# Kernel tuning notes

Hardware: AMD Instinct MI355X
Metric: run time of the kernel (lower is better)

Reference implementation:

```python
import jax, jax.numpy as jnp
import numpy as np

IN_SIZE = 784
Z_DIM = 128
K_DIM = 8192
BATCH = 16384
ENC_HIDDEN = [512, 256]          # EncoderMLP default
DEC_SIZES = [Z_DIM, 256, 512, 784]  # DecoderMLP default: [latent, *hidden]


def _linear(x, w, b):
    return x @ w + b


def find_nearest(query, target):
    # Faithful to: sqrt(sum((Q-T)^2, -1)).min(1)[1]; sqrt is monotone so
    # argmin of squared distance is identical. Computed via the GEMM
    # expansion instead of materializing the (N,K,D) broadcast tensor.
    q2 = jnp.sum(query * query, axis=1, keepdims=True)        # [N,1]
    t2 = jnp.sum(target * target, axis=1)                     # [K]
    d2 = q2 - 2.0 * (query @ target.T) + t2[None, :]          # [N,K]
    idx = jnp.argmin(d2, axis=1)
    return target[idx]


def setup_inputs() -> dict:
    key = jax.random.key(0)
    ks = jax.random.split(key, 16)
    s = 0.02
    inp = {"X": jax.random.uniform(ks[0], (BATCH, 1, 28, 28), dtype=jnp.float32)}
    # Encoder: 784 -> 512 -> 256 (mlp blocks, ReLU) -> 128 (plain Linear)
    enc_sizes = [IN_SIZE] + ENC_HIDDEN + [Z_DIM]
    for i, (din, dout) in enumerate(zip(enc_sizes, enc_sizes[1:]), 1):
        inp[f"enc_w{i}"] = s * jax.random.normal(ks[i], (din, dout), dtype=jnp.float32)
        inp[f"enc_b{i}"] = jnp.zeros((dout,), dtype=jnp.float32)
    # Codebook
    inp["codebook"] = jax.random.normal(ks[8], (K_DIM, Z_DIM), dtype=jnp.float32)
    # Decoder: 128 -> 256 -> 512 -> 784 (mlp blocks, ReLU) + sigmoid out
    for i, (din, dout) in enumerate(zip(DEC_SIZES, DEC_SIZES[1:]), 1):
        inp[f"dec_w{i}"] = s * jax.random.normal(ks[8 + i], (din, dout), dtype=jnp.float32)
        inp[f"dec_b{i}"] = jnp.zeros((dout,), dtype=jnp.float32)
    return inp


def reference(X, enc_w1, enc_b1, enc_w2, enc_b2, enc_w3, enc_b3, codebook,
              dec_w1, dec_b1, dec_w2, dec_b2, dec_w3, dec_b3):
    x = X.reshape(-1, IN_SIZE)
    # Encoder (mlp_block = Linear+ReLU, final layer plain Linear)
    h = jax.nn.relu(_linear(x, enc_w1, enc_b1))
    h = jax.nn.relu(_linear(h, enc_w2, enc_b2))
    z_enc = _linear(h, enc_w3, enc_b3)                         # [N, Z]
    # Nearest codebook vector for each encoding
    z_dec = find_nearest(z_enc, codebook)                      # [N, Z]
    # Decoder
    d = jax.nn.relu(_linear(z_dec, dec_w1, dec_b1))
    d = jax.nn.relu(_linear(d, dec_w2, dec_b2))
    d = jax.nn.relu(_linear(d, dec_w3, dec_b3))
    x_recon = jax.nn.sigmoid(d).reshape(-1, 1, 28, 28)
    # Nearest encoding for each codebook vector (for embedding loss)
    z_enc_for_embd = find_nearest(codebook, z_enc)             # [K, Z]
    return (x_recon, z_enc, z_dec, z_enc_for_embd)
```

## Files before the change

### kernel.cpp

```cpp
#include <hip/hip_runtime.h>
#include <math.h>

using u16 = unsigned short;
using u32 = unsigned int;
using u64 = unsigned long long;

typedef __bf16 bf16x8 __attribute__((ext_vector_type(8)));
typedef short  s16x8  __attribute__((ext_vector_type(8)));
typedef float  f32x4  __attribute__((ext_vector_type(4)));

__device__ __forceinline__ float b2f(u16 u){
  union { u32 i; float f; } x; x.i = ((u32)u) << 16; return x.f;
}
__device__ __forceinline__ u16 f2b(float f){
  union { float f; u32 i; } x; x.f = f;
  u32 i = x.i;
  u32 r = (i + 0x7fffu + ((i >> 16) & 1u)) >> 16;
  return (u16)r;
}
__device__ __forceinline__ f32x4 mfma16(s16x8 a, s16x8 b, f32x4 c){
  return __builtin_amdgcn_mfma_f32_16x16x32_bf16(
      __builtin_bit_cast(bf16x8, a), __builtin_bit_cast(bf16x8, b), c, 0, 0, 0);
}
__device__ __forceinline__ u64 shfl_xor_u64(u64 v, int m){
  int lo = __shfl_xor((int)(u32)v, m);
  int hi = __shfl_xor((int)(u32)(v >> 32), m);
  return ((u64)(u32)hi << 32) | (u32)lo;
}
__device__ __forceinline__ u64 umin64(u64 a, u64 b){ return a < b ? a : b; }
__device__ __forceinline__ u64 packmin(float v, int idx){
  u32 b = __float_as_uint(v);
  b = (b & 0x80000000u) ? ~b : (b | 0x80000000u);
  return ((u64)b << 32) | (u32)idx;
}
__device__ __forceinline__ void gload16(const void* g, void* l){
  __builtin_amdgcn_global_load_lds(
      (const __attribute__((address_space(1))) unsigned int*)g,
      (__attribute__((address_space(3))) unsigned int*)l, 16, 0, 0);
}

__global__ __launch_bounds__(256) void canary_k(float* out, float code){
  out[threadIdx.x] = code;
}

__global__ __launch_bounds__(256) void prep_weights(
    const float* __restrict__ w1, const float* __restrict__ w2, const float* __restrict__ w3,
    const float* __restrict__ dw1, const float* __restrict__ dw2, const float* __restrict__ dw3,
    const float* __restrict__ cb,
    u16* __restrict__ o1h, u16* __restrict__ o1l, u16* __restrict__ o2h, u16* __restrict__ o2l,
    u16* __restrict__ o3h, u16* __restrict__ o3l, u16* __restrict__ o4h, u16* __restrict__ o4l,
    u16* __restrict__ o5h, u16* __restrict__ o5l, u16* __restrict__ o6h, u16* __restrict__ o6l,
    u16* __restrict__ cbh, u16* __restrict__ cbl)
{
  size_t o = (size_t)blockIdx.x * 256 + threadIdx.x;
  if (o >= 1155072){
    size_t e = o - 1155072;
    if (e >= 1048576) return;
    float v = cb[e];
    u16 h = f2b(v);
    cbh[e] = h;
    cbl[e] = f2b(v - b2f(h));
    return;
  }
  const float* src; u16 *hi, *lo; int K, N, Kp; size_t base;
  if      (o <  425984){ src=w1;  hi=o1h; lo=o1l; K=784; N=512; Kp=832; base=0; }
  else if (o <  557056){ src=w2;  hi=o2h; lo=o2l; K=512; N=256; Kp=512; base=425984; }
  else if (o <  589824){ src=w3;  hi=o3h; lo=o3l; K=256; N=128; Kp=256; base=557056; }
  else if (o <  622592){ src=dw1; hi=o4h; lo=o4l; K=128; N=256; Kp=128; base=589824; }
  else if (o <  753664){ src=dw2; hi=o5h; lo=o5l; K=256; N=512; Kp=256; base=622592; }
  else                 { src=dw3; hi=o6h; lo=o6l; K=512; N=784; Kp=512; base=753664; }
  size_t e = o - base;
  int n = (int)(e / Kp), kp = (int)(e % Kp);
  u16 h = 0, l = 0;
  if (kp < K){
    float v = src[(size_t)kp * N + n];
    h = f2b(v);
    l = f2b(v - b2f(h));
  }
  hi[e] = h; lo[e] = l;
}

__device__ __forceinline__ void norm_row(const float* __restrict__ src, float* __restrict__ dst){
  const float4* r = (const float4*)src;
  float s = 0.f;
  for (int k = 0; k < 32; k++){
    float4 p = r[k];
    s += p.x * p.x + p.y * p.y + p.z * p.z + p.w * p.w;
  }
  *dst = s;
}

struct __align__(16) SmemGemm {
  u16 Ah[128][72];
  u16 Al[128][72];
  u16 Bh[128][72];
  u16 Bl[128][72];
};

template<int ACT, int OUTP>
__device__ __forceinline__ void gemm_body(
    SmemGemm& sm,
    const float* __restrict__ A, const u16* __restrict__ B0, const u16* __restrict__ B1,
    const float* __restrict__ bias, float* __restrict__ Cf,
    u16* __restrict__ P0, u16* __restrict__ P1,
    int Astr, int KLIM, int Kp, int KT, int N, int nRowsB, int bx, int by)
{
  const int tid = threadIdx.x;
  const int m0 = by * 128, n0 = bx * 128;
  const int wave = tid >> 6, lane = tid & 63;
  const int wm = (wave >> 1) * 64, wn = (wave & 1) * 64;
  const int quad = lane >> 4, l15 = lane & 15;
  f32x4 acc[4][4] = {};

  for (int kt = 0; kt < KT; ++kt){
    const int kb = kt * 64;
    #pragma unroll
    for (int c = 0; c < 8; c++){
      int idx = c * 256 + tid;
      int r = idx >> 4, c4 = (idx & 15) * 4;
      float4 v = make_float4(0.f, 0.f, 0.f, 0.f);
      if (kb + c4 < KLIM)
        v = *(const float4*)(A + (size_t)(m0 + r) * Astr + kb + c4);
      ushort4 h, l;
      h.x = f2b(v.x); l.x = f2b(v.x - b2f(h.x));
      h.y = f2b(v.y); l.y = f2b(v.y - b2f(h.y));
      h.z = f2b(v.z); l.z = f2b(v.z - b2f(h.z));
      h.w = f2b(v.w); l.w = f2b(v.w - b2f(h.w));
      *(ushort4*)&sm.Ah[r][c4] = h;
      *(ushort4*)&sm.Al[r][c4] = l;
    }
    #pragma unroll
    for (int c = 0; c < 4; c++){
      int idx = c * 256 + tid;
      int r = idx >> 3, col = (idx & 7) * 8;
      int rb = n0 + r; rb = rb < nRowsB ? rb : nRowsB - 1;
      *(uint4*)&sm.Bh[r][col] = *(const uint4*)(B0 + (size_t)rb * Kp + kb + col);
      *(uint4*)&sm.Bl[r][col] = *(const uint4*)(B1 + (size_t)rb * Kp + kb + col);
    }
    __syncthreads();
    #pragma unroll
    for (int kh = 0; kh < 2; ++kh){
      s16x8 ah[4], al[4], bh[4], bl[4];
      #pragma unroll
      for (int t4 = 0; t4 < 4; t4++){
        ah[t4] = *(const s16x8*)&sm.Ah[wm + t4 * 16 + l15][kh * 32 + quad * 8];
        al[t4] = *(const s16x8*)&sm.Al[wm + t4 * 16 + l15][kh * 32 + quad * 8];
        bh[t4] = *(const s16x8*)&sm.Bh[wn + t4 * 16 + l15][kh * 32 + quad * 8];
        bl[t4] = *(const s16x8*)&sm.Bl[wn + t4 * 16 + l15][kh * 32 + quad * 8];
      }
      #pragma unroll
      for (int mt = 0; mt < 4; mt++)
        #pragma unroll
        for (int nt = 0; nt < 4; nt++){
          acc[mt][nt] = mfma16(ah[mt], bh[nt], acc[mt][nt]);
          acc[mt][nt] = mfma16(ah[mt], bl[nt], acc[mt][nt]);
          acc[mt][nt] = mfma16(al[mt], bh[nt], acc[mt][nt]);
        }
    }
    __syncthreads();
  }

  float bvs[4]; int cols[4];
  #pragma unroll
  for (int nt = 0; nt < 4; nt++){
    int cN = n0 + wn + nt * 16 + l15;
    cols[nt] = cN;
    int cc = cN < N ? cN : N - 1;
    bvs[nt] = bias[cc];
  }
  #pragma unroll
  for (int mt = 0; mt < 4; mt++){
    int rbase = m0 + wm + mt * 16 + quad * 4;
    #pragma unroll
    for (int nt = 0; nt < 4; nt++){
      if (cols[nt] < N){
        #pragma unroll
        for (int r = 0; r < 4; r++){
          float v = acc[mt][nt][r] + bvs[nt];
          if (ACT >= 1) v = v > 0.f ? v : 0.f;
          if (ACT == 2) v = 1.f / (1.f + expf(-v));
          size_t off = (size_t)(rbase + r) * N + cols[nt];
          if (OUTP == 2){
            P0[off] = f2b(v);
          } else {
            Cf[off] = v;
            if (OUTP == 1){
              u16 h = f2b(v);
              P0[off] = h;
              P1[off] = f2b(v - b2f(h));
            }
          }
        }
      }
    }
  }
}

template<int ACT, int OUTP>
__global__ __launch_bounds__(256, 2) void gemm_k(
    const float* __restrict__ A, const u16* __restrict__ B0, const u16* __restrict__ B1,
    const float* __restrict__ bias, float* __restrict__ Cf,
    u16* __restrict__ P0, u16* __restrict__ P1,
    int Astr, int KLIM, int Kp, int KT, int N, int nRowsB)
{
  __shared__ SmemGemm sm;
  gemm_body<ACT, OUTP>(sm, A, B0, B1, bias, Cf, P0, P1, Astr, KLIM, Kp, KT, N, nRowsB,
                       blockIdx.x, blockIdx.y);
}

__global__ __launch_bounds__(256, 2) void fused1(
    const float* __restrict__ X,  const u16* __restrict__ W1h, const u16* __restrict__ W1l,
    const float* __restrict__ b1, float* __restrict__ h1,
    const float* __restrict__ cb, const u16* __restrict__ D1h, const u16* __restrict__ D1l,
    const float* __restrict__ db1, float* __restrict__ g1, float* __restrict__ t2f)
{
  __shared__ SmemGemm sm;
  int bid = blockIdx.x;
  if (bid < 512){
    gemm_body<1,0>(sm, X, W1h, W1l, b1, h1, nullptr, nullptr, 784, 784, 832, 13, 512, 512,
                   bid & 3, bid >> 2);
  } else if (bid < 640){
    int b = bid - 512;
    gemm_body<1,0>(sm, cb, D1h, D1l, db1, g1, nullptr, nullptr, 128, 128, 128, 2, 256, 256,
                   b & 1, b >> 1);
  } else {
    int r = (bid - 640) * 256 + threadIdx.x;
    norm_row(cb + (size_t)r * 128, t2f + r);
  }
}

__global__ __launch_bounds__(256, 2) void fused3(
    const float* __restrict__ h2, const u16* __restrict__ W3h, const u16* __restrict__ W3l,
    const float* __restrict__ b3, float* __restrict__ zenc,
    u16* __restrict__ zhi, u16* __restrict__ zlo,
    const float* __restrict__ g1, const u16* __restrict__ D2h, const u16* __restrict__ D2l,
    const float* __restrict__ db2, float* __restrict__ g2)
{
  __shared__ SmemGemm sm;
  int bid = blockIdx.x;
  if (bid < 128){
    gemm_body<0,1>(sm, h2, W3h, W3l, b3, zenc, zhi, zlo, 256, 256, 256, 4, 128, 128,
                   0, bid);
  } else {
    int b = bid - 128;
    gemm_body<1,0>(sm, g1, D2h, D2l, db2, g2, nullptr, nullptr, 256, 256, 256, 4, 512, 512,
                   b & 3, b >> 2);
  }
}

struct __align__(16) DistSmem {
  u16 smem[2][16384];
  u64 colbuf[4][128];
  u64 sRow[2][128];
  float q2s[128];
};

__device__ __forceinline__ void dist_body(
    DistSmem& sm,
    const u16* __restrict__ Zh, const u16* __restrict__ Zl,
    const u16* __restrict__ Bh, const u16* __restrict__ Bl,
    const float* __restrict__ zenc, const float* __restrict__ t2,
    u64* __restrict__ rowp, u64* __restrict__ colp, int strip, int iblk)
{
  const int tid = threadIdx.x;
  const int i0 = iblk * 128;
  const int wave = tid >> 6, lane = tid & 63;
  const int wm = (wave >> 1) * 32, wn = (wave & 1) * 64;
  const int quad = lane >> 4, l15 = lane & 15;

  const int swz = (l15 & 7) << 4;
  const int cof0 = (((quad << 4)     ) ^ swz) >> 1;
  const int cof1 = (((quad << 4) | 64) ^ swz) >> 1;

  if (tid < 128){
    norm_row(zenc + (size_t)(i0 + tid) * 128, &sm.q2s[tid]);
  }

  s16x8 zh[2][2][2], zl[2][2][2];
  #pragma unroll
  for (int kb = 0; kb < 2; kb++)
    #pragma unroll
    for (int kh = 0; kh < 2; kh++)
      #pragma unroll
      for (int mt = 0; mt < 2; mt++){
        size_t off = (size_t)(i0 + wm + mt * 16 + l15) * 128 + kb * 64 + kh * 32 + quad * 8;
        zh[kb][kh][mt] = *(const s16x8*)(Zh + off);
        zl[kb][kh][mt] = *(const s16x8*)(Zl + off);
      }

  #define STAGE(jt_, kb_, buf_) {                                              \
    size_t jb = (size_t)(strip * 2048 + (jt_) * 128) * 128 + (kb_) * 64;       \
    _Pragma("unroll")                                                          \
    for (int c = 0; c < 2; c++){                                               \
      int ci = c * 512 + tid;                                                  \
      int row = ci >> 3;                                                       \
      size_t g = jb + (size_t)row * 128 + (size_t)(((ci & 7) ^ (row & 7)) * 8);\
      u16* lp = &sm.smem[buf_][ci * 8];                                        \
      gload16(Bh + g, lp);                                                     \
      gload16(Bl + g, lp + 8192);                                              \
    }                                                                          \
  }

  #define COMPUTE(buf_, kb_) {                                                 \
    __builtin_amdgcn_s_setprio(1);                                             \
    _Pragma("unroll")                                                          \
    for (int kh = 0; kh < 2; kh++){                                            \
      const int cof = kh ? cof1 : cof0;                                        \
      s16x8 bh[4], bl[4];                                                      \
      _Pragma("unroll")                                                        \
      for (int nt = 0; nt < 4; nt++){                                          \
        int off = (wn + nt * 16 + l15) * 64 + cof;                             \
        bh[nt] = *(const s16x8*)&sm.smem[buf_][off];                           \
        bl[nt] = *(const s16x8*)&sm.smem[buf_][8192 + off];                    \
      }                                                                        \
      _Pragma("unroll")                                                        \
      for (int mt = 0; mt < 2; mt++)                                           \
        _Pragma("unroll")                                                      \
        for (int nt = 0; nt < 4; nt++){                                        \
          acc[mt][nt] = mfma16(zh[kb_][kh][mt], bh[nt], acc[mt][nt]);          \
          acc[mt][nt] = mfma16(zh[kb_][kh][mt], bl[nt], acc[mt][nt]);          \
          acc[mt][nt] = mfma16(zl[kb_][kh][mt], bh[nt], acc[mt][nt]);          \
          acc[mt][nt] = mfma16(zl[kb_][kh][mt], bl[nt], acc[mt][nt]);          \
        }                                                                      \
    }                                                                          \
    __builtin_amdgcn_s_setprio(0);                                             \
  }

  STAGE(0, 0, 0);

  asm volatile("s_waitcnt lgkmcnt(0)" ::: "memory");
  __builtin_amdgcn_s_barrier();

  float qv[2][4];
  #pragma unroll
  for (int mt = 0; mt < 2; mt++)
    #pragma unroll
    for (int r = 0; r < 4; r++)
      qv[mt][r] = sm.q2s[wm + mt * 16 + quad * 4 + r];

  u64 rowm[2][4];
  #pragma unroll
  for (int mt = 0; mt < 2; mt++)
    #pragma unroll
    for (int r = 0; r < 4; r++) rowm[mt][r] = ~0ULL;

  #pragma unroll 1
  for (int jt = 0; jt < 16; ++jt){
    const int j0 = strip * 2048 + jt * 128;
    float t2v[4]; int gj[4];
    #pragma unroll
    for (int nt = 0; nt < 4; nt++){
      gj[nt] = j0 + wn + nt * 16 + l15;
      t2v[nt] = t2[gj[nt]];
    }
    f32x4 acc[2][4] = {};

    STAGE(jt, 1, 1);
    asm volatile("s_waitcnt vmcnt(8)" ::: "memory");
    __builtin_amdgcn_s_barrier();
    COMPUTE(0, 0)
    __builtin_amdgcn_s_barrier();
    if (jt < 15){
      STAGE(jt + 1, 0, 0);
      asm volatile("s_waitcnt vmcnt(4)" ::: "memory");
    } else {
      asm volatile("s_waitcnt vmcnt(0)" ::: "memory");
    }
    __builtin_amdgcn_s_barrier();
    COMPUTE(1, 1)

    #pragma unroll
    for (int mt = 0; mt < 2; mt++){
      #pragma unroll
      for (int r = 0; r < 4; r++){
        float qq = qv[mt][r];
        float rbest = (qq - 2.f * acc[mt][0][r]) + t2v[0];
        int   ridx  = gj[0];
        #pragma unroll
        for (int nt = 1; nt < 4; nt++){
          float v = (qq - 2.f * acc[mt][nt][r]) + t2v[nt];
          if (v < rbest){ rbest = v; ridx = gj[nt]; }
        }
        rowm[mt][r] = umin64(rowm[mt][r], packmin(rbest, ridx));
      }
    }
    #pragma unroll
    for (int nt = 0; nt < 4; nt++){
      float cbest = 3.4e38f; int cidx = 0;
      #pragma unroll
      for (int mt = 0; mt < 2; mt++){
        #pragma unroll
        for (int r = 0; r < 4; r++){
          float vc = (t2v[nt] - 2.f * acc[mt][nt][r]) + qv[mt][r];
          if (vc < cbest){ cbest = vc; cidx = i0 + wm + mt * 16 + quad * 4 + r; }
        }
      }
      u64 p = packmin(cbest, cidx);
      p = umin64(p, shfl_xor_u64(p, 16));
      p = umin64(p, shfl_xor_u64(p, 32));
      if (quad == 0)
        sm.colbuf[wave >> 1][wn + nt * 16 + l15] = p;
    }
    __builtin_amdgcn_s_barrier();
    if (tid < 128){
      u64 p = umin64(umin64(sm.colbuf[0][tid], sm.colbuf[1][tid]),
                     umin64(sm.colbuf[2][tid], sm.colbuf[3][tid]));
      colp[(size_t)iblk * 8192 + j0 + tid] = p;
    }
  }
  #undef STAGE
  #undef COMPUTE

  #pragma unroll
  for (int mt = 0; mt < 2; mt++)
    #pragma unroll
    for (int r = 0; r < 4; r++){
      u64 p = rowm[mt][r];
      p = umin64(p, shfl_xor_u64(p, 1));
      p = umin64(p, shfl_xor_u64(p, 2));
      p = umin64(p, shfl_xor_u64(p, 4));
      p = umin64(p, shfl_xor_u64(p, 8));
      rowm[mt][r] = p;
    }
  if (l15 == 0){
    #pragma unroll
    for (int mt = 0; mt < 2; mt++)
      #pragma unroll
      for (int r = 0; r < 4; r++)
        sm.sRow[wave & 1][wm + mt * 16 + quad * 4 + r] = rowm[mt][r];
  }
  __syncthreads();
  if (tid < 128)
    rowp[(size_t)strip * 16384 + i0 + tid] = umin64(sm.sRow[0][tid], sm.sRow[1][tid]);
}

__global__ __launch_bounds__(512, 2) void dist_k(
    const u16* __restrict__ Zh, const u16* __restrict__ Zl,
    const u16* __restrict__ Bh, const u16* __restrict__ Bl,
    const float* __restrict__ zenc, const float* __restrict__ t2,
    u64* __restrict__ rowp, u64* __restrict__ colp)
{
  __shared__ DistSmem sm;
  dist_body(sm, Zh, Zl, Bh, Bl, zenc, t2, rowp, colp, blockIdx.x & 3, blockIdx.x >> 2);
}

union SmemF5 {
  SmemGemm g;
  struct { u64 s[4][64]; int sidx[64]; } r;
};

__global__ __launch_bounds__(256, 2) void fused5(
    const float* __restrict__ g2, const u16* __restrict__ D3h, const u16* __restrict__ D3l,
    const float* __restrict__ db3, u16* __restrict__ xdecb,
    const u64* __restrict__ rowp, const u64* __restrict__ colp,
    const float* __restrict__ cb, const float* __restrict__ zenc,
    float* __restrict__ zdec, float* __restrict__ zembd, int* __restrict__ rowidx)
{
  __shared__ SmemF5 sm;
  int bid = blockIdx.x;
  if (bid < 448){
    gemm_body<2,2>(sm.g, g2, D3h, D3l, db3, nullptr, xdecb, nullptr,
                   512, 512, 512, 8, 784, 784, bid % 7, bid / 7);
    return;
  }
  bid -= 448;
  int tid = threadIdx.x;
  if (bid < 256){
    int base = bid * 64;
    int n = base + (tid & 63);
    u64 best = ~0ULL;
    for (int p = tid >> 6; p < 4; p += 4)
      best = umin64(best, rowp[(size_t)p * 16384 + n]);
    sm.r.s[tid >> 6][tid & 63] = best;
    __syncthreads();
    if (tid < 64){
      u64 b = umin64(umin64(sm.r.s[0][tid], sm.r.s[1][tid]),
                     umin64(sm.r.s[2][tid], sm.r.s[3][tid]));
      int idx = (int)(b & 0xffffffffULL);
      idx = idx < 0 ? 0 : (idx > 8191 ? 8191 : idx);
      sm.r.sidx[tid] = idx;
      rowidx[base + tid] = idx;
    }
    __syncthreads();
    for (int q = 0; q < 32; q++){
      int e = q * 256 + tid; int r = e >> 7, c = e & 127;
      zdec[(size_t)(base + r) * 128 + c] = cb[(size_t)sm.r.sidx[r] * 128 + c];
    }
  } else {
    int base = (bid - 256) * 64;
    int n = base + (tid & 63);
    u64 best = ~0ULL;
    for (int p = tid >> 6; p < 128; p += 4)
      best = umin64(best, colp[(size_t)p * 8192 + n]);
    sm.r.s[tid >> 6][tid & 63] = best;
    __syncthreads();
    if (tid < 64){
      u64 b = umin64(umin64(sm.r.s[0][tid], sm.r.s[1][tid]),
                     umin64(sm.r.s[2][tid], sm.r.s[3][tid]));
      int idx = (int)(b & 0xffffffffULL);
      idx = idx < 0 ? 0 : (idx > 16383 ? 16383 : idx);
      sm.r.sidx[tid] = idx;
    }
    __syncthreads();
    for (int q = 0; q < 32; q++){
      int e = q * 256 + tid; int r = e >> 7, c = e & 127;
      zembd[(size_t)(base + r) * 128 + c] = zenc[(size_t)sm.r.sidx[r] * 128 + c];
    }
  }
}

__global__ __launch_bounds__(256) void gather_xrec(
    const u16* __restrict__ xdecb, const int* __restrict__ rowidx, float* __restrict__ xrec)
{
  size_t o = (size_t)blockIdx.x * 256 + threadIdx.x;
  int row = (int)(o / 784), c = (int)(o % 784);
  int idx = rowidx[row];
  idx = idx < 0 ? 0 : (idx > 8191 ? 8191 : idx);
  xrec[o] = b2f(xdecb[(size_t)idx * 784 + c]);
}

extern "C" void kernel_launch(void* const* d_in, const int* in_sizes, int n_in,
                              void* d_out, int out_size, void* d_ws, size_t ws_size,
                              hipStream_t stream){
  const float* X   = (const float*)d_in[0];
  const float* w1  = (const float*)d_in[1];  const float* b1  = (const float*)d_in[2];
  const float* w2  = (const float*)d_in[3];  const float* b2  = (const float*)d_in[4];
  const float* w3  = (const float*)d_in[5];  const float* b3  = (const float*)d_in[6];
  const float* cb  = (const float*)d_in[7];
  const float* dw1 = (const float*)d_in[8];  const float* db1 = (const float*)d_in[9];
  const float* dw2 = (const float*)d_in[10]; const float* db2 = (const float*)d_in[11];
  const float* dw3 = (const float*)d_in[12]; const float* db3 = (const float*)d_in[13];

  float* out   = (float*)d_out;
  float* xrec  = out;
  float* zenc  = out + 12845056;
  float* zdec  = zenc + 2097152;
  float* zembd = zdec + 2097152;

  const size_t NEEDED = 22020096;
  if (ws_size < NEEDED){
    canary_k<<<1, 256, 0, stream>>>(out, 1000.0f + (float)(ws_size >> 20));
    return;
  }

  char* ob = (char*)d_out;
  float* h1   = (float*)(ob + 0);
  u16*   zhi  = (u16*)(ob + 8388608);
  u16*   zlo  = (u16*)(ob + 12582912);
  float* g2   = (float*)(ob + 16777216);
  float* g1   = (float*)(ob + 33554432);
  u16*   cbhi = (u16*)(ob + 41943040);
  u16*   cblo = (u16*)(ob + 44040192);
  u64*   colp = (u64*)(ob + 0);

  char* w = (char*)d_ws;
  u16* W1Th = (u16*)(w + 0);        u16* W1Tl = (u16*)(w + 851968);
  u16* W2Th = (u16*)(w + 1703936);  u16* W2Tl = (u16*)(w + 1966080);
  u16* W3Th = (u16*)(w + 2228224);  u16* W3Tl = (u16*)(w + 2293760);
  u16* D1Th = (u16*)(w + 2359296);  u16* D1Tl = (u16*)(w + 2424832);
  u16* D2Th = (u16*)(w + 2490368);  u16* D2Tl = (u16*)(w + 2752512);
  u16* D3Th = (u16*)(w + 3014656);  u16* D3Tl = (u16*)(w + 3817472);
  float* t2f = (float*)(w + 4620288);
  int*  rowi = (int*)(w + 4653056);
  u64*  rowp = (u64*)(w + 4718592);
  float* h2  = (float*)(w + 5242880);
  u16* xdecb = (u16*)(w + 5242880);

  prep_weights<<<8608, 256, 0, stream>>>(w1, w2, w3, dw1, dw2, dw3, cb,
      W1Th, W1Tl, W2Th, W2Tl, W3Th, W3Tl, D1Th, D1Tl, D2Th, D2Tl, D3Th, D3Tl, cbhi, cblo);

  fused1<<<672, 256, 0, stream>>>(X, W1Th, W1Tl, b1, h1, cb, D1Th, D1Tl, db1, g1, t2f);

  gemm_k<1, 0><<<dim3(2, 128), 256, 0, stream>>>(h1, W2Th, W2Tl, b2, h2, nullptr, nullptr,
                                                 512, 512, 512, 8, 256, 256);

  fused3<<<384, 256, 0, stream>>>(h2, W3Th, W3Tl, b3, zenc, zhi, zlo,
                                  g1, D2Th, D2Tl, db2, g2);

  dist_k<<<512, 512, 0, stream>>>(zhi, zlo, cbhi, cblo, zenc, t2f, rowp, colp);

  fused5<<<832, 256, 0, stream>>>(g2, D3Th, D3Tl, db3, xdecb,
                                  rowp, colp, cb, zenc, zdec, zembd, rowi);

  gather_xrec<<<50176, 256, 0, stream>>>(xdecb, rowi, xrec);
}
```

Baseline: 500.1 us.

## Software-pipeline distance epilogue with next tile's MFMA using double accumulators

Splits the tile loop into a ping-pong schedule with two accumulator sets, so the row/column argmin scans for tile j are interleaved with the MFMA work for tile j+1. This is meant to hide the VALU-heavy epilogue (distance evaluation, packing, shuffles, LDS column merge) behind matrix-core work instead of running it serially after each tile. In exchange it doubles accumulator register use, which may raise VGPR pressure and lower occupancy. It also adds explicit prologue and epilogue code.

```diff
diff --git a/kernel.cpp b/kernel.cpp
--- a/kernel.cpp
+++ b/kernel.cpp
@@ -301,7 +301,7 @@
     }                                                                          \
   }
 
-  #define COMPUTE(buf_, kb_) {                                                 \
+  #define COMPUTE(buf_, kb_, ACC) {                                            \
     __builtin_amdgcn_s_setprio(1);                                             \
     _Pragma("unroll")                                                          \
     for (int kh = 0; kh < 2; kh++){                                            \
@@ -317,15 +317,72 @@
       for (int mt = 0; mt < 2; mt++)                                           \
         _Pragma("unroll")                                                      \
         for (int nt = 0; nt < 4; nt++){                                        \
-          acc[mt][nt] = mfma16(zh[kb_][kh][mt], bh[nt], acc[mt][nt]);          \
-          acc[mt][nt] = mfma16(zh[kb_][kh][mt], bl[nt], acc[mt][nt]);          \
-          acc[mt][nt] = mfma16(zl[kb_][kh][mt], bh[nt], acc[mt][nt]);          \
-          acc[mt][nt] = mfma16(zl[kb_][kh][mt], bl[nt], acc[mt][nt]);          \
+          ACC[mt][nt] = mfma16(zh[kb_][kh][mt], bh[nt], ACC[mt][nt]);          \
+          ACC[mt][nt] = mfma16(zh[kb_][kh][mt], bl[nt], ACC[mt][nt]);          \
+          ACC[mt][nt] = mfma16(zl[kb_][kh][mt], bh[nt], ACC[mt][nt]);          \
+          ACC[mt][nt] = mfma16(zl[kb_][kh][mt], bl[nt], ACC[mt][nt]);          \
         }                                                                      \
     }                                                                          \
     __builtin_amdgcn_s_setprio(0);                                             \
   }
 
+  #define LOADT2(T2V, J0_) {                                                   \
+    _Pragma("unroll")                                                          \
+    for (int nt = 0; nt < 4; nt++) T2V[nt] = t2[(J0_) + wn + nt * 16 + l15];   \
+  }
+
+  #define ZEROACC(ACC) {                                                       \
+    _Pragma("unroll")                                                          \
+    for (int mt = 0; mt < 2; mt++)                                             \
+      _Pragma("unroll")                                                        \
+      for (int nt = 0; nt < 4; nt++) ACC[mt][nt] = VZ;                         \
+  }
+
+  #define ROWSCAN(ACC, T2V, J0_) {                                             \
+    _Pragma("unroll")                                                          \
+    for (int mt = 0; mt < 2; mt++){                                            \
+      _Pragma("unroll")                                                        \
+      for (int r = 0; r < 4; r++){                                             \
+        float qq = qv[mt][r];                                                  \
+        float rbest = (qq - 2.f * ACC[mt][0][r]) + T2V[0];                     \
+        int   ridx  = (J0_) + wn + l15;                                        \
+        _Pragma("unroll")                                                      \
+        for (int nt = 1; nt < 4; nt++){                                        \
+          float v = (qq - 2.f * ACC[mt][nt][r]) + T2V[nt];                     \
+          if (v < rbest){ rbest = v; ridx = (J0_) + wn + nt * 16 + l15; }      \
+        }                                                                      \
+        rowm[mt][r] = umin64(rowm[mt][r], packmin(rbest, ridx));               \
+      }                                                                        \
+    }                                                                          \
+  }
+
+  #define COLSCAN(ACC, T2V) {                                                  \
+    _Pragma("unroll")                                                          \
+    for (int nt = 0; nt < 4; nt++){                                            \
+      float cbest = 3.4e38f; int cidx = 0;                                     \
+      _Pragma("unroll")                                                        \
+      for (int mt = 0; mt < 2; mt++){                                          \
+        _Pragma("unroll")                                                      \
+        for (int r = 0; r < 4; r++){                                           \
+          float vc = (T2V[nt] - 2.f * ACC[mt][nt][r]) + qv[mt][r];             \
+          if (vc < cbest){ cbest = vc; cidx = i0 + wm + mt * 16 + quad * 4 + r; } \
+        }                                                                      \
+      }                                                                        \
+      u64 p = packmin(cbest, cidx);                                            \
+      p = umin64(p, shfl_xor_u64(p, 16));                                      \
+      p = umin64(p, shfl_xor_u64(p, 32));                                      \
+      if (quad == 0) sm.colbuf[wave >> 1][wn + nt * 16 + l15] = p;             \
+    }                                                                          \
+  }
+
+  #define MERGECOL(J0_) {                                                      \
+    if (tid < 128){                                                            \
+      u64 p = umin64(umin64(sm.colbuf[0][tid], sm.colbuf[1][tid]),             \
+                     umin64(sm.colbuf[2][tid], sm.colbuf[3][tid]));            \
+      colp[(size_t)iblk * 8192 + (J0_) + tid] = p;                             \
+    }                                                                          \
+  }
+
   STAGE(0, 0, 0);
 
   asm volatile("s_waitcnt lgkmcnt(0)" ::: "memory");
@@ -344,72 +401,92 @@
     #pragma unroll
     for (int r = 0; r < 4; r++) rowm[mt][r] = ~0ULL;
 
+  const f32x4 VZ = {0.f, 0.f, 0.f, 0.f};
+  f32x4 accA[2][4], accB[2][4];
+  float t2vA[4], t2vB[4];
+  int j0A, j0B;
+
+  j0A = strip * 2048;
+  LOADT2(t2vA, j0A);
+  ZEROACC(accA);
+  STAGE(0, 1, 1);
+  asm volatile("s_waitcnt vmcnt(8)" ::: "memory");
+  __builtin_amdgcn_s_barrier();
+  COMPUTE(0, 0, accA)
+  __builtin_amdgcn_s_barrier();
+  STAGE(1, 0, 0);
+  asm volatile("s_waitcnt vmcnt(4)" ::: "memory");
+  __builtin_amdgcn_s_barrier();
+  COMPUTE(1, 1, accA)
+  __builtin_amdgcn_s_barrier();
+
   #pragma unroll 1
-  for (int jt = 0; jt < 16; ++jt){
-    const int j0 = strip * 2048 + jt * 128;
-    float t2v[4]; int gj[4];
-    #pragma unroll
-    for (int nt = 0; nt < 4; nt++){
-      gj[nt] = j0 + wn + nt * 16 + l15;
-      t2v[nt] = t2[gj[nt]];
-    }
-    f32x4 acc[2][4] = {};
-
-    STAGE(jt, 1, 1);
+  for (int jp = 0; jp < 7; ++jp){
+    const int jt1 = 2 * jp + 1;
+    j0B = strip * 2048 + jt1 * 128;
+    LOADT2(t2vB, j0B);
+    ZEROACC(accB);
+    STAGE(jt1, 1, 1);
     asm volatile("s_waitcnt vmcnt(8)" ::: "memory");
     __builtin_amdgcn_s_barrier();
-    COMPUTE(0, 0)
-    __builtin_amdgcn_s_barrier();
-    if (jt < 15){
-      STAGE(jt + 1, 0, 0);
-      asm volatile("s_waitcnt vmcnt(4)" ::: "memory");
-    } else {
-      asm volatile("s_waitcnt vmcnt(0)" ::: "memory");
-    }
-    __builtin_amdgcn_s_barrier();
-    COMPUTE(1, 1)
-
-    #pragma unroll
-    for (int mt = 0; mt < 2; mt++){
-      #pragma unroll
-      for (int r = 0; r < 4; r++){
-        float qq = qv[mt][r];
-        float rbest = (qq - 2.f * acc[mt][0][r]) + t2v[0];
-        int   ridx  = gj[0];
-        #pragma unroll
-        for (int nt = 1; nt < 4; nt++){
-          float v = (qq - 2.f * acc[mt][nt][r]) + t2v[nt];
-          if (v < rbest){ rbest = v; ridx = gj[nt]; }
-        }
-        rowm[mt][r] = umin64(rowm[mt][r], packmin(rbest, ridx));
-      }
-    }
-    #pragma unroll
-    for (int nt = 0; nt < 4; nt++){
-      float cbest = 3.4e38f; int cidx = 0;
-      #pragma unroll
-      for (int mt = 0; mt < 2; mt++){
-        #pragma unroll
-        for (int r = 0; r < 4; r++){
-          float vc = (t2v[nt] - 2.f * acc[mt][nt][r]) + qv[mt][r];
-          if (vc < cbest){ cbest = vc; cidx = i0 + wm + mt * 16 + quad * 4 + r; }
-        }
-      }
-      u64 p = packmin(cbest, cidx);
-      p = umin64(p, shfl_xor_u64(p, 16));
-      p = umin64(p, shfl_xor_u64(p, 32));
-      if (quad == 0)
-        sm.colbuf[wave >> 1][wn + nt * 16 + l15] = p;
-    }
-    __builtin_amdgcn_s_barrier();
-    if (tid < 128){
-      u64 p = umin64(umin64(sm.colbuf[0][tid], sm.colbuf[1][tid]),
-                     umin64(sm.colbuf[2][tid], sm.colbuf[3][tid]));
-      colp[(size_t)iblk * 8192 + j0 + tid] = p;
-    }
-  }
+    COMPUTE(0, 0, accB)
+    ROWSCAN(accA, t2vA, j0A)
+    __builtin_amdgcn_s_barrier();
+    STAGE(jt1 + 1, 0, 0);
+    asm volatile("s_waitcnt vmcnt(4)" ::: "memory");
+    __builtin_amdgcn_s_barrier();
+    COMPUTE(1, 1, accB)
+    COLSCAN(accA, t2vA)
+    __builtin_amdgcn_s_barrier();
+    MERGECOL(j0A)
+    const int jt2 = jt1 + 1;
+    j0A = strip * 2048 + jt2 * 128;
+    LOADT2(t2vA, j0A);
+    ZEROACC(accA);
+    STAGE(jt2, 1, 1);
+    asm volatile("s_waitcnt vmcnt(8)" ::: "memory");
+    __builtin_amdgcn_s_barrier();
+    COMPUTE(0, 0, accA)
+    ROWSCAN(accB, t2vB, j0B)
+    __builtin_amdgcn_s_barrier();
+    STAGE(jt2 + 1, 0, 0);
+    asm volatile("s_waitcnt vmcnt(4)" ::: "memory");
+    __builtin_amdgcn_s_barrier();
+    COMPUTE(1, 1, accA)
+    COLSCAN(accB, t2vB)
+    __builtin_amdgcn_s_barrier();
+    MERGECOL(j0B)
+  }
+
+  j0B = strip * 2048 + 15 * 128;
+  LOADT2(t2vB, j0B);
+  ZEROACC(accB);
+  STAGE(15, 1, 1);
+  asm volatile("s_waitcnt vmcnt(8)" ::: "memory");
+  __builtin_amdgcn_s_barrier();
+  COMPUTE(0, 0, accB)
+  ROWSCAN(accA, t2vA, j0A)
+  __builtin_amdgcn_s_barrier();
+  asm volatile("s_waitcnt vmcnt(0)" ::: "memory");
+  __builtin_amdgcn_s_barrier();
+  COMPUTE(1, 1, accB)
+  COLSCAN(accA, t2vA)
+  __builtin_amdgcn_s_barrier();
+  MERGECOL(j0A)
+
+  ROWSCAN(accB, t2vB, j0B)
+  __builtin_amdgcn_s_barrier();
+  COLSCAN(accB, t2vB)
+  __builtin_amdgcn_s_barrier();
+  MERGECOL(j0B)
+
   #undef STAGE
   #undef COMPUTE
+  #undef LOADT2
+  #undef ZEROACC
+  #undef ROWSCAN
+  #undef COLSCAN
+  #undef MERGECOL
 
   #pragma unroll
   for (int mt = 0; mt < 2; mt++)
```

New measurement: 632.0 us. 26.4% more time.
